# Performance work log

Measured on AMD Instinct MI355X. Metric: run time of the kernel, lower is better.

Reference implementation:

```python
import jax, jax.numpy as jnp
import numpy as np

B, N = 2, 512
CS, CZ = 384, 128
H, D, P, PV = 12, 16, 4, 8
W_C = (2.0 / (9.0 * P)) ** 0.5
W_L = (1.0 / 3.0) ** 0.5
CAT = H * CZ + H * D + H * PV * 3 + H * PV  # concat width into output linear


def setup_inputs() -> dict:
    key = jax.random.key(0)
    ks = jax.random.split(key, 14)
    sc = lambda n: np.float32(1.0 / np.sqrt(n))
    s_i = jax.random.normal(ks[0], (B, N, CS), jnp.float32)
    z_ij = jax.random.normal(ks[1], (B, N, N, CZ), jnp.float32)
    rots = jax.random.normal(ks[2], (B, N, 3, 3), jnp.float32)
    trans = jax.random.normal(ks[3], (B, N, 3), jnp.float32)
    wq = jax.random.normal(ks[4], (CS, H, D), jnp.float32) * sc(CS)
    wk = jax.random.normal(ks[5], (CS, H, D), jnp.float32) * sc(CS)
    wv = jax.random.normal(ks[6], (CS, H, D), jnp.float32) * sc(CS)
    wqp = jax.random.normal(ks[7], (CS, H, P, 3), jnp.float32) * sc(CS)
    wkp = jax.random.normal(ks[8], (CS, H, P, 3), jnp.float32) * sc(CS)
    wvp = jax.random.normal(ks[9], (CS, H, PV, 3), jnp.float32) * sc(CS)
    wb = jax.random.normal(ks[10], (CZ, H), jnp.float32) * sc(CZ)
    gamma = jax.random.normal(ks[11], (H,), jnp.float32)
    wout = jax.random.normal(ks[12], (CAT, CS), jnp.float32) * sc(CAT)
    bout = jnp.zeros((CS,), jnp.float32)
    return dict(s_i=s_i, z_ij=z_ij, rots=rots, trans=trans, wq=wq, wk=wk, wv=wv,
                wqp=wqp, wkp=wkp, wvp=wvp, wb=wb, gamma=gamma, wout=wout, bout=bout)


def reference(s_i, z_ij, rots, trans, wq, wk, wv, wqp, wkp, wvp, wb, gamma, wout, bout):
    # rigid apply: x_global = R @ x_local + t, per residue, broadcast over (h, p)
    def rig_apply(x):  # x: (b,i,h,p,3)
        return jnp.einsum('bixy,bihpy->bihpx', rots, x) + trans[:, :, None, None, :]

    def rig_invert_apply(x):  # R^T @ (x - t)
        return jnp.einsum('biyx,bihpy->bihpx', rots, x - trans[:, :, None, None, :])

    q = jnp.einsum('bic,chd->bihd', s_i, wq)
    k = jnp.einsum('bic,chd->bihd', s_i, wk)
    v = jnp.einsum('bic,chd->bihd', s_i, wv)
    qp = jnp.einsum('bic,chpx->bihpx', s_i, wqp)
    kp = jnp.einsum('bic,chpx->bihpx', s_i, wkp)
    vp = jnp.einsum('bic,chpx->bihpx', s_i, wvp)

    b_ij = jnp.einsum('bijc,ch->bijh', z_ij, wb)  # pair bias

    tq = rig_apply(qp)  # (b,i,h,p,3) in global frame
    tk = rig_apply(kp)
    # squared point distances summed over points: (b,i,j,h)
    d2 = jnp.sum((tq[:, :, None] - tk[:, None]) ** 2, axis=(-1, -2))

    a_s = jnp.einsum('bihd,bjhd->bijh', q, k) * np.float32(1.0 / np.sqrt(D))
    logits = W_L * (a_s + b_ij - (W_C * 0.5) * gamma * d2)
    a = jax.nn.softmax(logits, axis=2)  # softmax over j (dim=-2 of bijh)

    o_hat = jnp.einsum('bijh,bijd->bihd', a, z_ij)   # pair-value aggregation
    o = jnp.einsum('bijh,bjhd->bihd', a, v)          # scalar values
    tv = rig_apply(vp)                               # point values in global frame
    o_hp = rig_invert_apply(jnp.einsum('bijh,bjhpx->bihpx', a, tv))
    o_hp_norm = jnp.sqrt(jnp.sum(o_hp ** 2, axis=-1))  # (b,i,h,p)

    cat = jnp.concatenate([
        o_hat.reshape(B, N, H * CZ),
        o.reshape(B, N, H * D),
        o_hp.reshape(B, N, H * PV * 3),
        o_hp_norm.reshape(B, N, H * PV),
    ], axis=-1)
    return cat @ wout + bout
```

## Files before the change

kernel.cpp:

```cpp
#include <hip/hip_runtime.h>
#include <hip/hip_bf16.h>
#include <math.h>

#define BB 2
#define NN 512
#define CS 384
#define CZ 128
#define HH 12
#define CATW 2112

#define W_L_CONST 0.57735026919f
#define W_C_HALF 0.11785113019f
#define INV_SQRT_D 0.25f
#define LGP 516

__global__ void k_proj(const float* __restrict__ s_i,
                       const float* __restrict__ rots,
                       const float* __restrict__ trans,
                       const float* __restrict__ wq,
                       const float* __restrict__ wk,
                       const float* __restrict__ wv,
                       const float* __restrict__ wqp,
                       const float* __restrict__ wkp,
                       const float* __restrict__ wvp,
                       float* __restrict__ qw, float* __restrict__ kw,
                       float* __restrict__ vw, float* __restrict__ tqw,
                       float* __restrict__ tkw, float* __restrict__ tvw) {
  int t0 = blockIdx.x * 2;
  __shared__ float s_row[2][CS];
  __shared__ float praw[2][576];
  __shared__ float R[2][9], T[2][3];
  int tid = threadIdx.x;
  for (int idx = tid; idx < 2 * CS; idx += 256) {
    int tok = idx / CS, c = idx % CS;
    s_row[tok][c] = s_i[(size_t)(t0 + tok) * CS + c];
  }
  if (tid < 18) R[tid / 9][tid % 9] = rots[t0 * 9 + tid];
  if (tid < 6) T[tid / 3][tid % 3] = trans[t0 * 3 + tid];
  __syncthreads();

  for (int f = tid; f < 1152; f += 256) {
    const float* wp;
    int stride;
    if (f < 576) {
      int sel = f / 192, r = f % 192;
      wp = ((sel == 0) ? wq : (sel == 1) ? wk : wv) + r;
      stride = 192;
    } else {
      int g = f - 576;
      if (g < 144)      { wp = wqp + g;        stride = 144; }
      else if (g < 288) { wp = wkp + (g - 144); stride = 144; }
      else              { wp = wvp + (g - 288); stride = 288; }
    }
    float a0 = 0.f, a1 = 0.f;
    #pragma unroll 8
    for (int c = 0; c < CS; c++) {
      float w = wp[(size_t)c * stride];
      a0 += s_row[0][c] * w;
      a1 += s_row[1][c] * w;
    }
    if (f < 576) {
      int sel = f / 192, r = f % 192;
      float* dst = (sel == 0) ? qw : (sel == 1) ? kw : vw;
      dst[(size_t)(t0 + 0) * 192 + r] = a0;
      dst[(size_t)(t0 + 1) * 192 + r] = a1;
    } else {
      int g = f - 576;
      praw[0][g] = a0;
      praw[1][g] = a1;
    }
  }
  __syncthreads();
  for (int idx = tid; idx < 1152; idx += 256) {
    int tok = idx / 576, f = idx % 576;
    int base, r;
    float* dst;
    if (f < 144)      { r = f;       base = 0;   dst = tqw + (size_t)(t0 + tok) * 144; }
    else if (f < 288) { r = f - 144; base = 144; dst = tkw + (size_t)(t0 + tok) * 144; }
    else              { r = f - 288; base = 288; dst = tvw + (size_t)(t0 + tok) * 288; }
    int hp = r / 3, x = r % 3;
    float v0 = praw[tok][base + hp * 3 + 0];
    float v1 = praw[tok][base + hp * 3 + 1];
    float v2 = praw[tok][base + hp * 3 + 2];
    dst[r] = R[tok][x * 3 + 0] * v0 + R[tok][x * 3 + 1] * v1 + R[tok][x * 3 + 2] * v2 + T[tok][x];
  }
}

__global__ void k_bias(const float* __restrict__ z,
                       const float* __restrict__ wb,
                       float* __restrict__ bw) {
  __shared__ float zt[64][129];
  __shared__ float wbs[CZ * HH];
  __shared__ float bbs[64][12];
  int tid = threadIdx.x;
  int r0 = blockIdx.x * 64;
  int bi = r0 >> 9, j0 = r0 & 511;

  for (int idx = tid; idx < CZ * HH; idx += 256) wbs[idx] = wb[idx];
  const float* zbase = z + (size_t)r0 * CZ;
  for (int s = 0; s < 8; s++) {
    int idx = tid + s * 256;
    int row = idx >> 5, q = idx & 31;
    float4 v = *(const float4*)(zbase + (size_t)row * CZ + q * 4);
    zt[row][q * 4 + 0] = v.x;
    zt[row][q * 4 + 1] = v.y;
    zt[row][q * 4 + 2] = v.z;
    zt[row][q * 4 + 3] = v.w;
  }
  __syncthreads();

  int row = tid & 63, hbase = tid >> 6;
  float a0 = 0.f, a1 = 0.f, a2 = 0.f;
  #pragma unroll 8
  for (int c = 0; c < CZ; c++) {
    float zv = zt[row][c];
    a0 += zv * wbs[c * HH + hbase];
    a1 += zv * wbs[c * HH + hbase + 4];
    a2 += zv * wbs[c * HH + hbase + 8];
  }
  bbs[row][hbase] = a0;
  bbs[row][hbase + 4] = a1;
  bbs[row][hbase + 8] = a2;
  __syncthreads();

  for (int idx = tid; idx < 768; idx += 256) {
    int h = idx / 64, jl = idx % 64;
    bw[((size_t)bi * HH + h) * NN + j0 + jl] = bbs[jl][h];
  }
}

__global__ void k_att(const float* __restrict__ z,
                      const float* __restrict__ qw,
                      const float* __restrict__ kw,
                      const float* __restrict__ tqw,
                      const float* __restrict__ tkw,
                      const float* __restrict__ vw,
                      const float* __restrict__ tvw,
                      const float* __restrict__ gamma,
                      const float* __restrict__ rots,
                      const float* __restrict__ trans,
                      const float* __restrict__ bw,
                      float* __restrict__ catm) {
  int bi = blockIdx.x;
  int b = bi / NN;
  __shared__ float lg[HH][LGP];
  __shared__ float opart[4][480];
  __shared__ float qrow[192], tqrow[144], gam[HH];
  __shared__ float rm[HH][4], rs[HH][4];
  __shared__ float praw[288], ohp[288], R[9], T[3];
  int tid = threadIdx.x;
  int lane = tid & 63, wid = tid >> 6;

  const float* bwrow = bw + (size_t)bi * (HH * NN);
  for (int idx = tid; idx < HH * NN; idx += 256)
    lg[idx >> 9][idx & 511] = bwrow[idx];
  for (int idx = tid; idx < 192; idx += 256) qrow[idx] = qw[(size_t)bi * 192 + idx];
  if (tid < 144) tqrow[tid] = tqw[(size_t)bi * 144 + tid];
  if (tid < HH) gam[tid] = gamma[tid];
  if (tid < 9) R[tid] = rots[bi * 9 + tid];
  if (tid < 3) T[tid] = trans[bi * 3 + tid];
  __syncthreads();

  for (int s = 0; s < 24; s++) {
    int task = tid + s * 256;
    int j = task / 12, h = task % 12;
    const float4* kd = (const float4*)(kw + ((size_t)(b * NN + j)) * 192 + h * 16);
    float as = 0.f;
    #pragma unroll
    for (int q = 0; q < 4; q++) {
      float4 kv = kd[q];
      as += qrow[h * 16 + q * 4 + 0] * kv.x + qrow[h * 16 + q * 4 + 1] * kv.y +
            qrow[h * 16 + q * 4 + 2] * kv.z + qrow[h * 16 + q * 4 + 3] * kv.w;
    }
    const float4* td = (const float4*)(tkw + ((size_t)(b * NN + j)) * 144 + h * 12);
    float d2 = 0.f;
    #pragma unroll
    for (int q = 0; q < 3; q++) {
      float4 tv = td[q];
      float d0 = tqrow[h * 12 + q * 4 + 0] - tv.x;
      float d1 = tqrow[h * 12 + q * 4 + 1] - tv.y;
      float d2_ = tqrow[h * 12 + q * 4 + 2] - tv.z;
      float d3 = tqrow[h * 12 + q * 4 + 3] - tv.w;
      d2 += d0 * d0 + d1 * d1 + d2_ * d2_ + d3 * d3;
    }
    lg[h][j] = W_L_CONST * (as * INV_SQRT_D + lg[h][j] - W_C_HALF * gam[h] * d2);
  }
  __syncthreads();

  #pragma unroll
  for (int h = 0; h < HH; h++) {
    float m = fmaxf(lg[h][tid], lg[h][tid + 256]);
    #pragma unroll
    for (int off = 32; off >= 1; off >>= 1) m = fmaxf(m, __shfl_xor(m, off, 64));
    if (lane == 0) rm[h][wid] = m;
  }
  __syncthreads();
  #pragma unroll
  for (int h = 0; h < HH; h++) {
    float mx = fmaxf(fmaxf(rm[h][0], rm[h][1]), fmaxf(rm[h][2], rm[h][3]));
    float e0 = __expf(lg[h][tid] - mx);
    float e1 = __expf(lg[h][tid + 256] - mx);
    lg[h][tid] = e0;
    lg[h][tid + 256] = e1;
    float s = e0 + e1;
    #pragma unroll
    for (int off = 32; off >= 1; off >>= 1) s += __shfl_xor(s, off, 64);
    if (lane == 0) rs[h][wid] = s;
  }
  __syncthreads();
  #pragma unroll
  for (int h = 0; h < HH; h++) {
    float inv = 1.0f / (rs[h][0] + rs[h][1] + rs[h][2] + rs[h][3]);
    lg[h][tid] *= inv;
    lg[h][tid + 256] *= inv;
  }
  __syncthreads();

  float* crow = catm + (size_t)bi * CATW;
  int j0 = wid * 128;

  for (int t = lane; t < 480; t += 64) {
    const float* src;
    int h, str;
    if (t < 192) { h = t >> 4; src = vw + (size_t)b * NN * 192 + t; str = 192; }
    else { int f = t - 192; h = f / 24; src = tvw + (size_t)b * NN * 288 + f; str = 288; }
    float sum = 0.f;
    for (int jj = 0; jj < 128; jj += 4) {
      float4 av = *(const float4*)&lg[h][j0 + jj];
      sum += av.x * src[(size_t)(j0 + jj + 0) * str]
           + av.y * src[(size_t)(j0 + jj + 1) * str]
           + av.z * src[(size_t)(j0 + jj + 2) * str]
           + av.w * src[(size_t)(j0 + jj + 3) * str];
    }
    opart[wid][t] = sum;
  }
  __syncthreads();
  for (int t = tid; t < 480; t += 256) {
    float s = opart[0][t] + opart[1][t] + opart[2][t] + opart[3][t];
    if (t < 192) crow[1536 + t] = s;
    else praw[t - 192] = s;
  }
  __syncthreads();
  for (int f = tid; f < 288; f += 256) {
    int g = f / 3, x = f % 3;
    float v0 = praw[g * 3 + 0] - T[0];
    float v1 = praw[g * 3 + 1] - T[1];
    float v2 = praw[g * 3 + 2] - T[2];
    float val = R[0 * 3 + x] * v0 + R[1 * 3 + x] * v1 + R[2 * 3 + x] * v2;
    ohp[f] = val;
    crow[1728 + f] = val;
  }
  __syncthreads();
  if (tid < 96) {
    float x0 = ohp[tid * 3 + 0];
    float x1 = ohp[tid * 3 + 1];
    float x2 = ohp[tid * 3 + 2];
    crow[2016 + tid] = sqrtf(x0 * x0 + x1 * x1 + x2 * x2);
  }

  int hw = lane >> 5, c4 = (lane & 31) * 4;
  float4 acc[HH];
  #pragma unroll
  for (int h = 0; h < HH; h++) acc[h] = make_float4(0.f, 0.f, 0.f, 0.f);
  for (int stp = 0; stp < 64; stp++) {
    int j = j0 + stp * 2 + hw;
    float4 zv = *(const float4*)(z + ((size_t)bi * NN + j) * CZ + c4);
    #pragma unroll
    for (int h = 0; h < HH; h++) {
      float a = lg[h][j];
      acc[h].x += a * zv.x;
      acc[h].y += a * zv.y;
      acc[h].z += a * zv.z;
      acc[h].w += a * zv.w;
    }
  }
  __syncthreads();
  #pragma unroll
  for (int h = 0; h < HH; h++) {
    acc[h].x += __shfl_xor(acc[h].x, 32, 64);
    acc[h].y += __shfl_xor(acc[h].y, 32, 64);
    acc[h].z += __shfl_xor(acc[h].z, 32, 64);
    acc[h].w += __shfl_xor(acc[h].w, 32, 64);
  }
  float* pbuf = &lg[0][0];
  if (lane < 32) {
    #pragma unroll
    for (int h = 0; h < HH; h++)
      *(float4*)&pbuf[wid * 1536 + h * 128 + lane * 4] = acc[h];
  }
  __syncthreads();
  #pragma unroll
  for (int s = 0; s < 6; s++) {
    int idx = tid + s * 256;
    crow[idx] = pbuf[idx] + pbuf[1536 + idx] + pbuf[3072 + idx] + pbuf[4608 + idx];
  }
}

#define KCH 528
__global__ void k_gemm(const float* __restrict__ catm,
                       const float* __restrict__ wout,
                       float* __restrict__ pout) {
  __shared__ float As[16][68];
  __shared__ float Bs[16][64];
  int tid = threadIdx.x;
  int n0 = blockIdx.x * 64, m0 = blockIdx.y * 64, kbase = blockIdx.z * KCH;
  int tx = tid & 15, ty = tid >> 4;
  int sm = tid & 63, skk4 = tid >> 6;
  int bkk = tid >> 4, bn4 = (tid & 15) * 4;
  float acc[4][4] = {};
  for (int kt = 0; kt < KCH / 16; kt++) {
    int k0 = kbase + kt * 16;
    float4 ga = *(const float4*)(catm + (size_t)(m0 + sm) * CATW + k0 + skk4 * 4);
    float4 gb = *(const float4*)(wout + (size_t)(k0 + bkk) * 384 + n0 + bn4);
    __syncthreads();
    As[skk4 * 4 + 0][sm] = ga.x;
    As[skk4 * 4 + 1][sm] = ga.y;
    As[skk4 * 4 + 2][sm] = ga.z;
    As[skk4 * 4 + 3][sm] = ga.w;
    *(float4*)&Bs[bkk][bn4] = gb;
    __syncthreads();
    #pragma unroll
    for (int kk = 0; kk < 16; kk++) {
      float4 av = *(const float4*)&As[kk][ty * 4];
      float4 bv = *(const float4*)&Bs[kk][tx * 4];
      acc[0][0] += av.x * bv.x; acc[0][1] += av.x * bv.y; acc[0][2] += av.x * bv.z; acc[0][3] += av.x * bv.w;
      acc[1][0] += av.y * bv.x; acc[1][1] += av.y * bv.y; acc[1][2] += av.y * bv.z; acc[1][3] += av.y * bv.w;
      acc[2][0] += av.z * bv.x; acc[2][1] += av.z * bv.y; acc[2][2] += av.z * bv.z; acc[2][3] += av.z * bv.w;
      acc[3][0] += av.w * bv.x; acc[3][1] += av.w * bv.y; acc[3][2] += av.w * bv.z; acc[3][3] += av.w * bv.w;
    }
  }
  float* pdst = pout + (size_t)blockIdx.z * (1024 * 384);
  #pragma unroll
  for (int mm = 0; mm < 4; mm++) {
    *(float4*)&pdst[(size_t)(m0 + ty * 4 + mm) * 384 + n0 + tx * 4] =
        make_float4(acc[mm][0], acc[mm][1], acc[mm][2], acc[mm][3]);
  }
}

__global__ void k_red(const float* __restrict__ pout,
                      const float* __restrict__ bout,
                      float* __restrict__ out) {
  int idx = blockIdx.x * 256 + threadIdx.x;
  const int TOTAL = 1024 * 384;
  float s = pout[idx] + pout[TOTAL + idx] + pout[2 * TOTAL + idx] + pout[3 * TOTAL + idx];
  out[idx] = s + bout[idx % 384];
}

extern "C" void kernel_launch(void* const* d_in, const int* in_sizes, int n_in,
                              void* d_out, int out_size, void* d_ws, size_t ws_size,
                              hipStream_t stream) {
  const float* s_i   = (const float*)d_in[0];
  const float* z     = (const float*)d_in[1];
  const float* rots  = (const float*)d_in[2];
  const float* trans = (const float*)d_in[3];
  const float* wq    = (const float*)d_in[4];
  const float* wk    = (const float*)d_in[5];
  const float* wv    = (const float*)d_in[6];
  const float* wqp   = (const float*)d_in[7];
  const float* wkp   = (const float*)d_in[8];
  const float* wvp   = (const float*)d_in[9];
  const float* wb    = (const float*)d_in[10];
  const float* gamma = (const float*)d_in[11];
  const float* wout  = (const float*)d_in[12];
  const float* bout  = (const float*)d_in[13];
  float* out = (float*)d_out;

  float* ws = (float*)d_ws;
  const size_t TOK = (size_t)BB * NN;
  float* qw  = ws;
  float* kw  = qw + TOK * 192;
  float* vw  = kw + TOK * 192;
  float* tqw = vw + TOK * 192;
  float* tkw = tqw + TOK * 144;
  float* tvw = tkw + TOK * 144;
  float* bw  = tvw + TOK * 288;
  float* catm = bw + TOK * HH * NN;
  float* pout = catm + TOK * CATW;

  k_proj<<<BB * NN / 2, 256, 0, stream>>>(s_i, rots, trans, wq, wk, wv, wqp, wkp, wvp,
                                          qw, kw, vw, tqw, tkw, tvw);
  k_bias<<<BB * NN * NN / 64, 256, 0, stream>>>(z, wb, bw);
  k_att<<<BB * NN, 256, 0, stream>>>(z, qw, kw, tqw, tkw, vw, tvw, gamma, rots, trans,
                                     bw, catm);
  dim3 gg(6, 16, 4);
  k_gemm<<<gg, 256, 0, stream>>>(catm, wout, pout);
  k_red<<<(1024 * 384) / 256, 256, 0, stream>>>(pout, bout, out);
}
```

Baseline: 704.4 us.

## Restructure pair-bias kernel and transpose attention weights for z aggregation

The pair-bias kernel now gives each wavefront 64 rows of z. It stages 32-column chunks through per-wave shared memory, keeps all 12 head accumulators in registers and reads wb straight from global (uniform, cached), so each block covers four times the rows. In the attention kernel, the normalized weights are transposed into a j-major scratch buffer, so one float4 read yields several heads. The z-aggregation loop also loads four z rows per iteration for more memory-level parallelism. The costs are an extra transpose pass with a sync, higher register pressure, and reuse of shared scratch space across phases.

After: 767.4 us. +8.9%, slower.

```diff
diff --git a/kernel.cpp b/kernel.cpp
--- a/kernel.cpp
+++ b/kernel.cpp
@@ -89,44 +89,41 @@
 __global__ void k_bias(const float* __restrict__ z,
                        const float* __restrict__ wb,
                        float* __restrict__ bw) {
-  __shared__ float zt[64][129];
-  __shared__ float wbs[CZ * HH];
-  __shared__ float bbs[64][12];
-  int tid = threadIdx.x;
-  int r0 = blockIdx.x * 64;
-  int bi = r0 >> 9, j0 = r0 & 511;
-
-  for (int idx = tid; idx < CZ * HH; idx += 256) wbs[idx] = wb[idx];
-  const float* zbase = z + (size_t)r0 * CZ;
-  for (int s = 0; s < 8; s++) {
-    int idx = tid + s * 256;
-    int row = idx >> 5, q = idx & 31;
-    float4 v = *(const float4*)(zbase + (size_t)row * CZ + q * 4);
-    zt[row][q * 4 + 0] = v.x;
-    zt[row][q * 4 + 1] = v.y;
-    zt[row][q * 4 + 2] = v.z;
-    zt[row][q * 4 + 3] = v.w;
-  }
-  __syncthreads();
-
-  int row = tid & 63, hbase = tid >> 6;
-  float a0 = 0.f, a1 = 0.f, a2 = 0.f;
-  #pragma unroll 8
-  for (int c = 0; c < CZ; c++) {
-    float zv = zt[row][c];
-    a0 += zv * wbs[c * HH + hbase];
-    a1 += zv * wbs[c * HH + hbase + 4];
-    a2 += zv * wbs[c * HH + hbase + 8];
-  }
-  bbs[row][hbase] = a0;
-  bbs[row][hbase + 4] = a1;
-  bbs[row][hbase + 8] = a2;
-  __syncthreads();
-
-  for (int idx = tid; idx < 768; idx += 256) {
-    int h = idx / 64, jl = idx % 64;
-    bw[((size_t)bi * HH + h) * NN + j0 + jl] = bbs[jl][h];
-  }
+  __shared__ float zt[4][64][33];
+  int tid = threadIdx.x, lane = tid & 63, w = tid >> 6;
+  int bi = blockIdx.x >> 1;
+  int j0 = (blockIdx.x & 1) * 256 + w * 64;
+  const float* zbase = z + ((size_t)bi * NN + j0) * CZ;
+
+  float acc[12];
+  #pragma unroll
+  for (int h = 0; h < 12; h++) acc[h] = 0.f;
+
+  for (int cc = 0; cc < 4; cc++) {
+    int c0 = cc * 32;
+    #pragma unroll
+    for (int i = 0; i < 8; i++) {
+      int row = i * 8 + (lane >> 3), cq = lane & 7;
+      float4 v = *(const float4*)(zbase + (size_t)row * CZ + c0 + cq * 4);
+      *(float4*)&zt[w][row][cq * 4] = v;
+    }
+    #pragma unroll
+    for (int c = 0; c < 32; c += 4) {
+      float4 zv = *(const float4*)&zt[w][lane][c];
+      const float* w0 = wb + (size_t)(c0 + c) * HH;
+      #pragma unroll
+      for (int h = 0; h < 12; h++) acc[h] += zv.x * w0[h];
+      #pragma unroll
+      for (int h = 0; h < 12; h++) acc[h] += zv.y * w0[12 + h];
+      #pragma unroll
+      for (int h = 0; h < 12; h++) acc[h] += zv.z * w0[24 + h];
+      #pragma unroll
+      for (int h = 0; h < 12; h++) acc[h] += zv.w * w0[36 + h];
+    }
+  }
+  #pragma unroll
+  for (int h = 0; h < 12; h++)
+    bw[((size_t)bi * HH + h) * NN + j0 + lane] = acc[h];
 }
 
 __global__ void k_att(const float* __restrict__ z,
@@ -144,10 +141,10 @@
   int bi = blockIdx.x;
   int b = bi / NN;
   __shared__ float lg[HH][LGP];
-  __shared__ float opart[4][480];
+  __shared__ float scratch[6144];
   __shared__ float qrow[192], tqrow[144], gam[HH];
   __shared__ float rm[HH][4], rs[HH][4];
-  __shared__ float praw[288], ohp[288], R[9], T[3];
+  __shared__ float R[9], T[3];
   int tid = threadIdx.x;
   int lane = tid & 63, wid = tid >> 6;
 
@@ -218,6 +215,9 @@
 
   float* crow = catm + (size_t)bi * CATW;
   int j0 = wid * 128;
+  float* opart = scratch;
+  float* praw = scratch + 1920;
+  float* ohp  = scratch + 2208;
 
   for (int t = lane; t < 480; t += 64) {
     const float* src;
@@ -232,11 +232,11 @@
            + av.z * src[(size_t)(j0 + jj + 2) * str]
            + av.w * src[(size_t)(j0 + jj + 3) * str];
     }
-    opart[wid][t] = sum;
+    opart[wid * 480 + t] = sum;
   }
   __syncthreads();
   for (int t = tid; t < 480; t += 256) {
-    float s = opart[0][t] + opart[1][t] + opart[2][t] + opart[3][t];
+    float s = opart[t] + opart[480 + t] + opart[960 + t] + opart[1440 + t];
     if (t < 192) crow[1536 + t] = s;
     else praw[t - 192] = s;
   }
@@ -257,21 +257,43 @@
     float x2 = ohp[tid * 3 + 2];
     crow[2016 + tid] = sqrtf(x0 * x0 + x1 * x1 + x2 * x2);
   }
+  __syncthreads();
+
+  for (int idx = tid; idx < 6144; idx += 256) {
+    int j = idx / 12, h = idx - j * 12;
+    scratch[idx] = lg[h][j];
+  }
+  __syncthreads();
 
   int hw = lane >> 5, c4 = (lane & 31) * 4;
   float4 acc[HH];
   #pragma unroll
   for (int h = 0; h < HH; h++) acc[h] = make_float4(0.f, 0.f, 0.f, 0.f);
-  for (int stp = 0; stp < 64; stp++) {
-    int j = j0 + stp * 2 + hw;
-    float4 zv = *(const float4*)(z + ((size_t)bi * NN + j) * CZ + c4);
-    #pragma unroll
-    for (int h = 0; h < HH; h++) {
-      float a = lg[h][j];
-      acc[h].x += a * zv.x;
-      acc[h].y += a * zv.y;
-      acc[h].z += a * zv.z;
-      acc[h].w += a * zv.w;
+  const float* zr = z + (size_t)bi * NN * CZ;
+  for (int stp = 0; stp < 16; stp++) {
+    int jb = j0 + stp * 8;
+    float4 zv[4];
+    #pragma unroll
+    for (int u = 0; u < 4; u++)
+      zv[u] = *(const float4*)(zr + (size_t)(jb + 2 * u + hw) * CZ + c4);
+    #pragma unroll
+    for (int u = 0; u < 4; u++) {
+      int j = jb + 2 * u + hw;
+      float4 A0 = *(const float4*)&scratch[j * 12];
+      float4 A1 = *(const float4*)&scratch[j * 12 + 4];
+      float4 A2 = *(const float4*)&scratch[j * 12 + 8];
+      acc[0].x += A0.x * zv[u].x; acc[0].y += A0.x * zv[u].y; acc[0].z += A0.x * zv[u].z; acc[0].w += A0.x * zv[u].w;
+      acc[1].x += A0.y * zv[u].x; acc[1].y += A0.y * zv[u].y; acc[1].z += A0.y * zv[u].z; acc[1].w += A0.y * zv[u].w;
+      acc[2].x += A0.z * zv[u].x; acc[2].y += A0.z * zv[u].y; acc[2].z += A0.z * zv[u].z; acc[2].w += A0.z * zv[u].w;
+      acc[3].x += A0.w * zv[u].x; acc[3].y += A0.w * zv[u].y; acc[3].z += A0.w * zv[u].z; acc[3].w += A0.w * zv[u].w;
+      acc[4].x += A1.x * zv[u].x; acc[4].y += A1.x * zv[u].y; acc[4].z += A1.x * zv[u].z; acc[4].w += A1.x * zv[u].w;
+      acc[5].x += A1.y * zv[u].x; acc[5].y += A1.y * zv[u].y; acc[5].z += A1.y * zv[u].z; acc[5].w += A1.y * zv[u].w;
+      acc[6].x += A1.z * zv[u].x; acc[6].y += A1.z * zv[u].y; acc[6].z += A1.z * zv[u].z; acc[6].w += A1.z * zv[u].w;
+      acc[7].x += A1.w * zv[u].x; acc[7].y += A1.w * zv[u].y; acc[7].z += A1.w * zv[u].z; acc[7].w += A1.w * zv[u].w;
+      acc[8].x += A2.x * zv[u].x; acc[8].y += A2.x * zv[u].y; acc[8].z += A2.x * zv[u].z; acc[8].w += A2.x * zv[u].w;
+      acc[9].x += A2.y * zv[u].x; acc[9].y += A2.y * zv[u].y; acc[9].z += A2.y * zv[u].z; acc[9].w += A2.y * zv[u].w;
+      acc[10].x += A2.z * zv[u].x; acc[10].y += A2.z * zv[u].y; acc[10].z += A2.z * zv[u].z; acc[10].w += A2.z * zv[u].w;
+      acc[11].x += A2.w * zv[u].x; acc[11].y += A2.w * zv[u].y; acc[11].z += A2.w * zv[u].z; acc[11].w += A2.w * zv[u].w;
     }
   }
   __syncthreads();
@@ -286,7 +308,7 @@
   if (lane < 32) {
     #pragma unroll
     for (int h = 0; h < HH; h++)
-      *(float4*)&pbuf[wid * 1536 + h * 128 + lane * 4] = acc[h];
+      *(float4*)&pbuf[wid * 1536 + h * 128 + (lane & 31) * 4] = acc[h];
   }
   __syncthreads();
   #pragma unroll
@@ -379,7 +401,7 @@
 
   k_proj<<<BB * NN / 2, 256, 0, stream>>>(s_i, rots, trans, wq, wk, wv, wqp, wkp, wvp,
                                           qw, kw, vw, tqw, tkw, tvw);
-  k_bias<<<BB * NN * NN / 64, 256, 0, stream>>>(z, wb, bw);
+  k_bias<<<BB * NN * NN / 256, 256, 0, stream>>>(z, wb, bw);
   k_att<<<BB * NN, 256, 0, stream>>>(z, qw, kw, tqw, tkw, vw, tvw, gamma, rots, trans,
                                      bw, catm);
   dim3 gg(6, 16, 4);
```
